# Performance work log

Measured on AMD Instinct MI355X. Metric: run time of the kernel, lower is better.

The kernel has to match this reference:

```python
import jax, jax.numpy as jnp
import numpy as np
from jax import lax

INPUT_SIZE = 128
HIDDEN = 2048
OUTPUT = 1
SEQ_LEN = 4096


def setup_inputs() -> dict:
    key = jax.random.key(0)
    ks = jax.random.split(key, 8)
    s = 0.05
    return {
        "input_seq": jax.random.normal(ks[0], (SEQ_LEN, INPUT_SIZE), dtype=jnp.float32),
        "W_ih": jax.random.normal(ks[1], (4 * HIDDEN, INPUT_SIZE), dtype=jnp.float32) * s,
        "W_hh": jax.random.normal(ks[2], (4 * HIDDEN, HIDDEN), dtype=jnp.float32) * s,
        "b_ih": jax.random.normal(ks[3], (4 * HIDDEN,), dtype=jnp.float32) * s,
        "b_hh": jax.random.normal(ks[4], (4 * HIDDEN,), dtype=jnp.float32) * s,
        "W_lin": jax.random.normal(ks[5], (OUTPUT, HIDDEN), dtype=jnp.float32) * s,
        "b_lin": jax.random.normal(ks[6], (OUTPUT,), dtype=jnp.float32) * s,
    }


def reference(input_seq, W_ih, W_hh, b_ih, b_hh, W_lin, b_lin):
    H = W_hh.shape[1]
    # Pre-project all timesteps through the input weights: [L, 4H]
    gx = input_seq @ W_ih.T + (b_ih + b_hh)

    def step(carry, g_x):
        h, c = carry
        gates = g_x + h @ W_hh.T  # [4H], PyTorch gate order i,f,g,o
        i = jax.nn.sigmoid(gates[0 * H:1 * H])
        f = jax.nn.sigmoid(gates[1 * H:2 * H])
        g = jnp.tanh(gates[2 * H:3 * H])
        o = jax.nn.sigmoid(gates[3 * H:4 * H])
        c_new = f * c + i * g
        h_new = o * jnp.tanh(c_new)
        return (h_new, c_new), None

    h0 = jnp.zeros((H,), dtype=input_seq.dtype)
    c0 = jnp.zeros((H,), dtype=input_seq.dtype)
    (h_last, _), _ = lax.scan(step, (h0, c0), gx)
    # predictions[-1] == linear(lstm_out[-1]) since the head is per-timestep
    return h_last @ W_lin.T + b_lin
```

## Files before the change

### kernel.cpp

```cpp
#include <hip/hip_runtime.h>
#include <stdint.h>


#define SEQ   4096
#define NIN   128
#define HID   2048
#define NBLK  256
#define NTHR  512

typedef unsigned int u32x4 __attribute__((ext_vector_type(4)));

__device__ __forceinline__ uint64_t ld8_sys(const void* p) {
  uint64_t r;
  asm volatile("global_load_dwordx2 %0, %1, off sc0 sc1\n\t"
               "s_waitcnt vmcnt(0)"
               : "=v"(r) : "v"(p) : "memory");
  return r;
}
__device__ __forceinline__ void st4_sys(void* p, uint32_t v) {
  asm volatile("global_store_dword %0, %1, off sc0 sc1"
               :: "v"(p), "v"(v) : "memory");
}
__device__ __forceinline__ void st8_sys(void* p, uint64_t v) {
  asm volatile("global_store_dwordx2 %0, %1, off sc0 sc1"
               :: "v"(p), "v"(v) : "memory");
}

__device__ __forceinline__ uint32_t f32_to_f16lo(float x) {
  uint32_t r;
  asm("v_cvt_f16_f32 %0, %1" : "=v"(r) : "v"(x));
  return r & 0xFFFFu;
}
__device__ __forceinline__ float f16lo_to_f32(uint32_t u) {
  float r;
  asm("v_cvt_f32_f16 %0, %1" : "=v"(r) : "v"(u));
  return r;
}

template <int CTRL>
__device__ __forceinline__ float dpp_add(float x) {
  int y = __builtin_amdgcn_update_dpp(0, __float_as_int(x), CTRL, 0xF, 0xF, true);
  return x + __int_as_float(y);
}
__device__ __forceinline__ float wave_reduce(float x) {
  x = dpp_add<0x111>(x);
  x = dpp_add<0x112>(x);
  x = dpp_add<0x114>(x);
  x = dpp_add<0x118>(x);
  x = dpp_add<0x142>(x);
  x = dpp_add<0x143>(x);
  return x;
}

__device__ __forceinline__ float fast_sigmoid(float x) {
  return 1.0f / (1.0f + __expf(-x));
}
__device__ __forceinline__ float fast_tanh(float x) {
  return 1.0f - 2.0f / (1.0f + __expf(2.0f * x));
}

__global__ __launch_bounds__(NTHR, 2) void lstm_persist(
    const float* __restrict__ X, const float* __restrict__ Wih,
    const float* __restrict__ Whh, const float* __restrict__ bih,
    const float* __restrict__ bhh, const float* __restrict__ Wlin,
    const float* __restrict__ blin, float* __restrict__ out,
    uint32_t* __restrict__ ws) {
  const int tid = threadIdx.x;
  const int blk = blockIdx.x;
  const int w   = tid >> 6;
  const int l   = tid & 63;

  uint32_t* hslots = ws;
  uint64_t* fbuf   = (uint64_t*)(ws + 2 * HID);

  __shared__ __align__(16) float h_lds[2][HID];
  volatile __shared__ uint32_t pub_lds[8];
  __shared__ float red[8];
  __shared__ float fin[NBLK];

  if (w == 0) __builtin_amdgcn_s_setprio(2);

  float whh[4][32];
  float wih[4][2];
  float bias4[4];
#pragma unroll
  for (int G = 0; G < 4; ++G) {
    const size_t Rg = (size_t)(G * HID + blk * 8 + w);
    const float4* src = (const float4*)(Whh + Rg * HID + l * 32);
#pragma unroll
    for (int m = 0; m < 8; ++m) {
      float4 v = src[m];
      whh[G][m * 4 + 0] = v.x; whh[G][m * 4 + 1] = v.y;
      whh[G][m * 4 + 2] = v.z; whh[G][m * 4 + 3] = v.w;
    }
    wih[G][0] = Wih[Rg * NIN + l * 2 + 0];
    wih[G][1] = Wih[Rg * NIN + l * 2 + 1];
    bias4[G]  = bih[Rg] + bhh[Rg];
  }
  const float wlin = Wlin[blk * 8 + w];

  if (tid < 8) {
    st4_sys(&hslots[0 * HID + blk * 8 + tid], 0u);
    st4_sys(&hslots[1 * HID + blk * 8 + tid], 0xFFFF0000u);
    pub_lds[tid] = 0xFFFF0000u;
  }
  if (tid == 0)
    st8_sys(&fbuf[blk], 0xFFFFFFFF00000000ull);
  __syncthreads();

  float cc = 0.0f;
  float hl = 0.0f;

  float xp0 = X[(size_t)0 * NIN + l * 2 + 0];
  float xp1 = X[(size_t)0 * NIN + l * 2 + 1];

  for (int t = 1; t <= SEQ; ++t) {
    const uint32_t want16 = (uint32_t)(t - 1) & 0xFFFFu;
    const int par = (t - 1) & 1;
    const float x0 = xp0, x1 = xp1;

    if (w == 0) {
      const char* base = (const char*)(hslots + (size_t)par * HID) + l * 16;
      const char* p0 = base;
      const char* p1 = base + 4096;
      u32x4 a0, a1, a2, a3, a4, a5, a6, a7;
      for (;;) {
        asm volatile(
            "global_load_dwordx4 %0, %8, off sc0 sc1\n\t"
            "global_load_dwordx4 %1, %8, off offset:1024 sc0 sc1\n\t"
            "global_load_dwordx4 %2, %8, off offset:2048 sc0 sc1\n\t"
            "global_load_dwordx4 %3, %8, off offset:3072 sc0 sc1\n\t"
            "global_load_dwordx4 %4, %9, off sc0 sc1\n\t"
            "global_load_dwordx4 %5, %9, off offset:1024 sc0 sc1\n\t"
            "global_load_dwordx4 %6, %9, off offset:2048 sc0 sc1\n\t"
            "global_load_dwordx4 %7, %9, off offset:3072 sc0 sc1\n\t"
            "s_waitcnt vmcnt(0)"
            : "=v"(a0), "=v"(a1), "=v"(a2), "=v"(a3),
              "=v"(a4), "=v"(a5), "=v"(a6), "=v"(a7)
            : "v"(p0), "v"(p1) : "memory");
        bool ok = true;
#define CK4(A) ok &= ((A[0] >> 16) == want16) & ((A[1] >> 16) == want16) && \
                     ((A[2] >> 16) == want16) & ((A[3] >> 16) == want16);
        CK4(a0) CK4(a1) CK4(a2) CK4(a3) CK4(a4) CK4(a5) CK4(a6) CK4(a7)
#undef CK4
        if (__all(ok)) break;
        __builtin_amdgcn_s_sleep(1);
      }
      const int lsw = l ^ (l >> 3);
#define FAN(A, K)                                                   \
      {                                                             \
        float4 hw;                                                  \
        hw.x = f16lo_to_f32(A[0] & 0xFFFFu);                        \
        hw.y = f16lo_to_f32(A[1] & 0xFFFFu);                        \
        hw.z = f16lo_to_f32(A[2] & 0xFFFFu);                        \
        hw.w = f16lo_to_f32(A[3] & 0xFFFFu);                        \
        *(float4*)&h_lds[par][(64 * K + lsw) * 4] = hw;             \
      }
      FAN(a0, 0) FAN(a1, 1) FAN(a2, 2) FAN(a3, 3)
      FAN(a4, 4) FAN(a5, 5) FAN(a6, 6) FAN(a7, 7)
#undef FAN
    }
    __syncthreads();

    {
      const int tn = (t < SEQ) ? t : SEQ - 1;
      xp0 = X[(size_t)tn * NIN + l * 2 + 0];
      xp1 = X[(size_t)tn * NIN + l * 2 + 1];
    }

    const float* hb = h_lds[par];
    float acc0 = 0.f, acc1 = 0.f, acc2 = 0.f, acc3 = 0.f;
#pragma unroll
    for (int i = 0; i < 8; ++i) {
      const int uu = l * 8 + i;
      const int ph = uu ^ ((uu >> 3) & 7);
      const float4 hv = *(const float4*)&hb[ph * 4];
      acc0 = fmaf(whh[0][i * 4 + 0], hv.x, acc0);
      acc0 = fmaf(whh[0][i * 4 + 1], hv.y, acc0);
      acc0 = fmaf(whh[0][i * 4 + 2], hv.z, acc0);
      acc0 = fmaf(whh[0][i * 4 + 3], hv.w, acc0);
      acc1 = fmaf(whh[1][i * 4 + 0], hv.x, acc1);
      acc1 = fmaf(whh[1][i * 4 + 1], hv.y, acc1);
      acc1 = fmaf(whh[1][i * 4 + 2], hv.z, acc1);
      acc1 = fmaf(whh[1][i * 4 + 3], hv.w, acc1);
      acc2 = fmaf(whh[2][i * 4 + 0], hv.x, acc2);
      acc2 = fmaf(whh[2][i * 4 + 1], hv.y, acc2);
      acc2 = fmaf(whh[2][i * 4 + 2], hv.z, acc2);
      acc2 = fmaf(whh[2][i * 4 + 3], hv.w, acc2);
      acc3 = fmaf(whh[3][i * 4 + 0], hv.x, acc3);
      acc3 = fmaf(whh[3][i * 4 + 1], hv.y, acc3);
      acc3 = fmaf(whh[3][i * 4 + 2], hv.z, acc3);
      acc3 = fmaf(whh[3][i * 4 + 3], hv.w, acc3);
    }
    acc0 = fmaf(wih[0][0], x0, acc0); acc0 = fmaf(wih[0][1], x1, acc0);
    acc1 = fmaf(wih[1][0], x0, acc1); acc1 = fmaf(wih[1][1], x1, acc1);
    acc2 = fmaf(wih[2][0], x0, acc2); acc2 = fmaf(wih[2][1], x1, acc2);
    acc3 = fmaf(wih[3][0], x0, acc3); acc3 = fmaf(wih[3][1], x1, acc3);

    acc0 = wave_reduce(acc0);
    acc1 = wave_reduce(acc1);
    acc2 = wave_reduce(acc2);
    acc3 = wave_reduce(acc3);

    if (l == 63) {
      const float i_ = fast_sigmoid(acc0 + bias4[0]);
      const float f_ = fast_sigmoid(acc1 + bias4[1]);
      const float g_ = fast_tanh(acc2 + bias4[2]);
      const float o_ = fast_sigmoid(acc3 + bias4[3]);
      cc = fmaf(f_, cc, i_ * g_);
      const float h = o_ * fast_tanh(cc);
      hl = h;
      pub_lds[w] = ((uint32_t)t << 16) | f32_to_f16lo(h);
    }
    if (w == 0 && l < 8) {
      uint32_t v;
      do { v = pub_lds[l]; } while ((v >> 16) != (uint32_t)t);
      st4_sys(&hslots[(size_t)(t & 1) * HID + blk * 8 + l], v);
    }
  }

  if (l == 63) red[w] = hl * wlin;
  __syncthreads();
  if (tid == 0) {
    float s = red[0] + red[1] + red[2] + red[3] +
              red[4] + red[5] + red[6] + red[7];
    uint64_t pv = (uint64_t)__float_as_uint(s) |
                  ((uint64_t)(uint32_t)(SEQ + 1) << 32);
    st8_sys(&fbuf[blk], pv);
  }
  if (blk == 0) {
    if (tid < NBLK) {
      uint64_t v;
      do {
        v = ld8_sys(&fbuf[tid]);
      } while ((uint32_t)(v >> 32) != (uint32_t)(SEQ + 1));
      fin[tid] = __uint_as_float((uint32_t)v);
    }
    __syncthreads();
    if (tid == 0) {
      float s = blin[0];
      for (int i = 0; i < NBLK; ++i) s += fin[i];
      out[0] = s;
    }
  }
}

extern "C" void kernel_launch(void* const* d_in, const int* in_sizes, int n_in,
                              void* d_out, int out_size, void* d_ws,
                              size_t ws_size, hipStream_t stream) {
  const float* X    = (const float*)d_in[0];
  const float* Wih  = (const float*)d_in[1];
  const float* Whh  = (const float*)d_in[2];
  const float* bih  = (const float*)d_in[3];
  const float* bhh  = (const float*)d_in[4];
  const float* Wlin = (const float*)d_in[5];
  const float* blin = (const float*)d_in[6];
  float* out   = (float*)d_out;
  uint32_t* ws = (uint32_t*)d_ws;

  void* args[] = {(void*)&X,    (void*)&Wih,  (void*)&Whh,
                  (void*)&bih,  (void*)&bhh,  (void*)&Wlin,
                  (void*)&blin, (void*)&out,  (void*)&ws};
  hipLaunchCooperativeKernel((const void*)lstm_persist, dim3(NBLK), dim3(NTHR),
                             args, 0, stream);
}
```

Measured before the change: 9.177 ms.

## Store recurrent weights as packed fp16 and use dot2 with fewer, larger blocks

Recurrent weights are converted to packed fp16 pairs held in registers, and the matvec uses fdot2 on packed fp16 hidden state kept in LDS instead of fp32 FMAs. Halving the register footprint allows 1024-thread blocks, with 16 units per block across 128 blocks, so fewer blocks take part in the cross-block handoff each step. The intent is to cut per-step ALU and LDS work and reduce synchronisation participants. In exchange, weights and the hidden-state products lose precision, and per-block publish work grows.

```diff
diff --git a/kernel.cpp b/kernel.cpp
--- a/kernel.cpp
+++ b/kernel.cpp
@@ -5,10 +5,12 @@
 #define SEQ   4096
 #define NIN   128
 #define HID   2048
-#define NBLK  256
-#define NTHR  512
+#define NBLK  128
+#define NTHR  1024
+#define UPB   16
 
 typedef unsigned int u32x4 __attribute__((ext_vector_type(4)));
+typedef _Float16 half2_t __attribute__((ext_vector_type(2)));
 
 __device__ __forceinline__ uint64_t ld8_sys(const void* p) {
   uint64_t r;
@@ -35,6 +37,27 @@
   float r;
   asm("v_cvt_f32_f16 %0, %1" : "=v"(r) : "v"(u));
   return r;
+}
+__device__ __forceinline__ uint32_t pack_f16x2(float a, float b) {
+  return f32_to_f16lo(a) | (f32_to_f16lo(b) << 16);
+}
+__device__ __forceinline__ half2_t as_h2(uint32_t u) {
+  union { uint32_t u; half2_t h; } x; x.u = u; return x.h;
+}
+
+#if defined(__has_builtin)
+#if __has_builtin(__builtin_amdgcn_fdot2)
+#define HAVE_FDOT2 1
+#endif
+#endif
+__device__ __forceinline__ float dot2(uint32_t w, uint32_t h, float acc) {
+#ifdef HAVE_FDOT2
+  return __builtin_amdgcn_fdot2(as_h2(w), as_h2(h), acc, false);
+#else
+  acc = fmaf(f16lo_to_f32(w & 0xFFFFu), f16lo_to_f32(h & 0xFFFFu), acc);
+  acc = fmaf(f16lo_to_f32(w >> 16),     f16lo_to_f32(h >> 16),     acc);
+  return acc;
+#endif
 }
 
 template <int CTRL>
@@ -59,7 +82,34 @@
   return 1.0f - 2.0f / (1.0f + __expf(2.0f * x));
 }
 
-__global__ __launch_bounds__(NTHR, 2) void lstm_persist(
+__device__ __forceinline__ int qpos(int q) { return q ^ ((q >> 3) & 7); }
+
+__device__ __forceinline__ bool poll8(const char* p0, const char* p1,
+                                      u32x4& a0, u32x4& a1, u32x4& a2, u32x4& a3,
+                                      u32x4& a4, u32x4& a5, u32x4& a6, u32x4& a7,
+                                      uint32_t want16) {
+  asm volatile(
+      "global_load_dwordx4 %0, %8, off sc0 sc1\n\t"
+      "global_load_dwordx4 %1, %8, off offset:1024 sc0 sc1\n\t"
+      "global_load_dwordx4 %2, %8, off offset:2048 sc0 sc1\n\t"
+      "global_load_dwordx4 %3, %8, off offset:3072 sc0 sc1\n\t"
+      "global_load_dwordx4 %4, %9, off sc0 sc1\n\t"
+      "global_load_dwordx4 %5, %9, off offset:1024 sc0 sc1\n\t"
+      "global_load_dwordx4 %6, %9, off offset:2048 sc0 sc1\n\t"
+      "global_load_dwordx4 %7, %9, off offset:3072 sc0 sc1\n\t"
+      "s_waitcnt vmcnt(0)"
+      : "=v"(a0), "=v"(a1), "=v"(a2), "=v"(a3),
+        "=v"(a4), "=v"(a5), "=v"(a6), "=v"(a7)
+      : "v"(p0), "v"(p1) : "memory");
+  bool ok = true;
+#define CK4(A) ok &= ((A[0] >> 16) == want16) & ((A[1] >> 16) == want16) && \
+                     ((A[2] >> 16) == want16) & ((A[3] >> 16) == want16);
+  CK4(a0) CK4(a1) CK4(a2) CK4(a3) CK4(a4) CK4(a5) CK4(a6) CK4(a7)
+#undef CK4
+  return __all(ok) != 0;
+}
+
+__global__ __launch_bounds__(NTHR, 4) void lstm_persist(
     const float* __restrict__ X, const float* __restrict__ Wih,
     const float* __restrict__ Whh, const float* __restrict__ bih,
     const float* __restrict__ bhh, const float* __restrict__ Wlin,
@@ -73,35 +123,35 @@
   uint32_t* hslots = ws;
   uint64_t* fbuf   = (uint64_t*)(ws + 2 * HID);
 
-  __shared__ __align__(16) float h_lds[2][HID];
-  volatile __shared__ uint32_t pub_lds[8];
-  __shared__ float red[8];
+  __shared__ __align__(16) uint32_t hp_lds[2][1024];
+  volatile __shared__ uint32_t pub_lds[UPB];
+  __shared__ float red[UPB];
   __shared__ float fin[NBLK];
 
   if (w == 0) __builtin_amdgcn_s_setprio(2);
 
-  float whh[4][32];
+  uint32_t whh[4][16];
   float wih[4][2];
   float bias4[4];
 #pragma unroll
   for (int G = 0; G < 4; ++G) {
-    const size_t Rg = (size_t)(G * HID + blk * 8 + w);
+    const size_t Rg = (size_t)(G * HID + blk * UPB + w);
     const float4* src = (const float4*)(Whh + Rg * HID + l * 32);
 #pragma unroll
     for (int m = 0; m < 8; ++m) {
       float4 v = src[m];
-      whh[G][m * 4 + 0] = v.x; whh[G][m * 4 + 1] = v.y;
-      whh[G][m * 4 + 2] = v.z; whh[G][m * 4 + 3] = v.w;
+      whh[G][m * 2 + 0] = pack_f16x2(v.x, v.y);
+      whh[G][m * 2 + 1] = pack_f16x2(v.z, v.w);
     }
     wih[G][0] = Wih[Rg * NIN + l * 2 + 0];
     wih[G][1] = Wih[Rg * NIN + l * 2 + 1];
     bias4[G]  = bih[Rg] + bhh[Rg];
   }
-  const float wlin = Wlin[blk * 8 + w];
-
-  if (tid < 8) {
-    st4_sys(&hslots[0 * HID + blk * 8 + tid], 0u);
-    st4_sys(&hslots[1 * HID + blk * 8 + tid], 0xFFFF0000u);
+  const float wlin = Wlin[blk * UPB + w];
+
+  if (tid < UPB) {
+    st4_sys(&hslots[0 * HID + blk * UPB + tid], 0u);
+    st4_sys(&hslots[1 * HID + blk * UPB + tid], 0xFFFF0000u);
     pub_lds[tid] = 0xFFFF0000u;
   }
   if (tid == 0)
@@ -120,41 +170,19 @@
     const float x0 = xp0, x1 = xp1;
 
     if (w == 0) {
-      const char* base = (const char*)(hslots + (size_t)par * HID) + l * 16;
-      const char* p0 = base;
-      const char* p1 = base + 4096;
+      const char* hp = (const char*)(hslots + (size_t)par * HID) + l * 16;
       u32x4 a0, a1, a2, a3, a4, a5, a6, a7;
-      for (;;) {
-        asm volatile(
-            "global_load_dwordx4 %0, %8, off sc0 sc1\n\t"
-            "global_load_dwordx4 %1, %8, off offset:1024 sc0 sc1\n\t"
-            "global_load_dwordx4 %2, %8, off offset:2048 sc0 sc1\n\t"
-            "global_load_dwordx4 %3, %8, off offset:3072 sc0 sc1\n\t"
-            "global_load_dwordx4 %4, %9, off sc0 sc1\n\t"
-            "global_load_dwordx4 %5, %9, off offset:1024 sc0 sc1\n\t"
-            "global_load_dwordx4 %6, %9, off offset:2048 sc0 sc1\n\t"
-            "global_load_dwordx4 %7, %9, off offset:3072 sc0 sc1\n\t"
-            "s_waitcnt vmcnt(0)"
-            : "=v"(a0), "=v"(a1), "=v"(a2), "=v"(a3),
-              "=v"(a4), "=v"(a5), "=v"(a6), "=v"(a7)
-            : "v"(p0), "v"(p1) : "memory");
-        bool ok = true;
-#define CK4(A) ok &= ((A[0] >> 16) == want16) & ((A[1] >> 16) == want16) && \
-                     ((A[2] >> 16) == want16) & ((A[3] >> 16) == want16);
-        CK4(a0) CK4(a1) CK4(a2) CK4(a3) CK4(a4) CK4(a5) CK4(a6) CK4(a7)
-#undef CK4
-        if (__all(ok)) break;
+      while (!poll8(hp, hp + 4096, a0, a1, a2, a3, a4, a5, a6, a7, want16))
         __builtin_amdgcn_s_sleep(1);
-      }
-      const int lsw = l ^ (l >> 3);
-#define FAN(A, K)                                                   \
-      {                                                             \
-        float4 hw;                                                  \
-        hw.x = f16lo_to_f32(A[0] & 0xFFFFu);                        \
-        hw.y = f16lo_to_f32(A[1] & 0xFFFFu);                        \
-        hw.z = f16lo_to_f32(A[2] & 0xFFFFu);                        \
-        hw.w = f16lo_to_f32(A[3] & 0xFFFFu);                        \
-        *(float4*)&h_lds[par][(64 * K + lsw) * 4] = hw;             \
+      const int qbase = l >> 1;
+      const int woff  = (l & 1) * 2;
+#define FAN(A, K)                                                     \
+      {                                                               \
+        uint32_t pp0 = (A[0] & 0xFFFFu) | (A[1] << 16);               \
+        uint32_t pp1 = (A[2] & 0xFFFFu) | (A[3] << 16);               \
+        const int q = 32 * K + qbase;                                 \
+        uint2 pv; pv.x = pp0; pv.y = pp1;                             \
+        *(uint2*)&hp_lds[par][qpos(q) * 4 + woff] = pv;               \
       }
       FAN(a0, 0) FAN(a1, 1) FAN(a2, 2) FAN(a3, 3)
       FAN(a4, 4) FAN(a5, 5) FAN(a6, 6) FAN(a7, 7)
@@ -168,29 +196,20 @@
       xp1 = X[(size_t)tn * NIN + l * 2 + 1];
     }
 
-    const float* hb = h_lds[par];
+    const uint32_t* hq = hp_lds[par];
     float acc0 = 0.f, acc1 = 0.f, acc2 = 0.f, acc3 = 0.f;
 #pragma unroll
-    for (int i = 0; i < 8; ++i) {
-      const int uu = l * 8 + i;
-      const int ph = uu ^ ((uu >> 3) & 7);
-      const float4 hv = *(const float4*)&hb[ph * 4];
-      acc0 = fmaf(whh[0][i * 4 + 0], hv.x, acc0);
-      acc0 = fmaf(whh[0][i * 4 + 1], hv.y, acc0);
-      acc0 = fmaf(whh[0][i * 4 + 2], hv.z, acc0);
-      acc0 = fmaf(whh[0][i * 4 + 3], hv.w, acc0);
-      acc1 = fmaf(whh[1][i * 4 + 0], hv.x, acc1);
-      acc1 = fmaf(whh[1][i * 4 + 1], hv.y, acc1);
-      acc1 = fmaf(whh[1][i * 4 + 2], hv.z, acc1);
-      acc1 = fmaf(whh[1][i * 4 + 3], hv.w, acc1);
-      acc2 = fmaf(whh[2][i * 4 + 0], hv.x, acc2);
-      acc2 = fmaf(whh[2][i * 4 + 1], hv.y, acc2);
-      acc2 = fmaf(whh[2][i * 4 + 2], hv.z, acc2);
-      acc2 = fmaf(whh[2][i * 4 + 3], hv.w, acc2);
-      acc3 = fmaf(whh[3][i * 4 + 0], hv.x, acc3);
-      acc3 = fmaf(whh[3][i * 4 + 1], hv.y, acc3);
-      acc3 = fmaf(whh[3][i * 4 + 2], hv.z, acc3);
-      acc3 = fmaf(whh[3][i * 4 + 3], hv.w, acc3);
+    for (int i4 = 0; i4 < 4; ++i4) {
+      const int q = (l << 2) | i4;
+      const u32x4 hv = *(const u32x4*)&hq[qpos(q) * 4];
+#pragma unroll
+      for (int jj = 0; jj < 4; ++jj) {
+        const int p = i4 * 4 + jj;
+        acc0 = dot2(whh[0][p], hv[jj], acc0);
+        acc1 = dot2(whh[1][p], hv[jj], acc1);
+        acc2 = dot2(whh[2][p], hv[jj], acc2);
+        acc3 = dot2(whh[3][p], hv[jj], acc3);
+      }
     }
     acc0 = fmaf(wih[0][0], x0, acc0); acc0 = fmaf(wih[0][1], x1, acc0);
     acc1 = fmaf(wih[1][0], x0, acc1); acc1 = fmaf(wih[1][1], x1, acc1);
@@ -212,18 +231,19 @@
       hl = h;
       pub_lds[w] = ((uint32_t)t << 16) | f32_to_f16lo(h);
     }
-    if (w == 0 && l < 8) {
+    if (w == 0 && l < UPB) {
       uint32_t v;
       do { v = pub_lds[l]; } while ((v >> 16) != (uint32_t)t);
-      st4_sys(&hslots[(size_t)(t & 1) * HID + blk * 8 + l], v);
+      st4_sys(&hslots[(size_t)(t & 1) * HID + blk * UPB + l], v);
     }
   }
 
   if (l == 63) red[w] = hl * wlin;
   __syncthreads();
   if (tid == 0) {
-    float s = red[0] + red[1] + red[2] + red[3] +
-              red[4] + red[5] + red[6] + red[7];
+    float s = 0.0f;
+#pragma unroll
+    for (int i = 0; i < UPB; ++i) s += red[i];
     uint64_t pv = (uint64_t)__float_as_uint(s) |
                   ((uint64_t)(uint32_t)(SEQ + 1) << 32);
     st8_sys(&fbuf[blk], pv);
```

Result: slower. 14.04 ms (+53.0%).
